# Optimization experiments

Measured on AMD Instinct MI355X. Metric: run time of the kernel, lower is better.

## Reference

```python
import jax, jax.numpy as jnp
from jax import lax
import numpy as np

B, H, T = 16, 1024, 1500
K = 3               # conv kernel size
MAX_TOK = 192       # max_decode_tokens (static padded token dim)
TEMP = 0.35
LLW = 0.25          # length_loss_weight
EPS = 1e-6


def setup_inputs() -> dict:
    key = jax.random.key(0)
    ks = jax.random.split(key, 8)
    encoder_outputs = jax.random.normal(ks[0], (B, H, T), dtype=jnp.float32)
    encoder_lengths = jax.random.randint(ks[1], (B,), 0, T)
    target_token_lengths = jax.random.randint(ks[2], (B,), 0, MAX_TOK)
    conv_w = jax.random.normal(ks[3], (H, H, K), dtype=jnp.float32) * 0.02  # OIH
    conv_b = jax.random.normal(ks[4], (H,), dtype=jnp.float32) * 0.02
    proj_w = jax.random.normal(ks[5], (H,), dtype=jnp.float32) * 0.02      # Linear(H,1)
    proj_b = jax.random.normal(ks[6], (), dtype=jnp.float32) * 0.02
    return {
        "encoder_outputs": encoder_outputs,
        "encoder_lengths": encoder_lengths,
        "target_token_lengths": target_token_lengths,
        "conv_w": conv_w,
        "conv_b": conv_b,
        "proj_w": proj_w,
        "proj_b": proj_b,
    }


def reference(encoder_outputs, encoder_lengths, target_token_lengths,
              conv_w, conv_b, proj_w, proj_b):
    b, h, t = encoder_outputs.shape
    dt = encoder_outputs.dtype

    # temporal conv (same padding), channel-first
    conv = lax.conv_general_dilated(
        encoder_outputs, conv_w, window_strides=(1,), padding="SAME",
        dimension_numbers=("NCH", "OIH", "NCH")) + conv_b[None, :, None]
    conv_feat = conv.transpose(0, 2, 1)  # [B,T,H]

    # softplus(Linear(silu(conv_feat))) + 1e-4  -> raw weights [B,T]
    raw = jax.nn.softplus(
        jnp.einsum("bth,h->bt", jax.nn.silu(conv_feat), proj_w) + proj_b) + 1e-4

    time_mask = (jnp.arange(t)[None, :] < encoder_lengths[:, None]).astype(dt)
    raw = raw * time_mask
    raw_mass = raw.sum(axis=1)  # [B]

    tok_len = jnp.clip(target_token_lengths, 1, MAX_TOK)
    alignment_loss = jnp.mean(jnp.abs(raw_mass - tok_len.astype(dt))) * LLW

    # vectorized (masked) version of the per-sample loop, padded to MAX_TOK
    scale = tok_len.astype(dt) / jnp.maximum(raw_mass, EPS)          # [B]
    sw = raw * scale[:, None]                                        # scaled weights [B,T]
    centers = jnp.cumsum(sw, axis=1) - 0.5 * sw                      # [B,T]
    token_centers = jnp.arange(MAX_TOK, dtype=dt) + 0.5              # [K]
    dist = centers[:, :, None] - token_centers[None, None, :]        # [B,T,K]
    assign = jnp.exp(-(dist * dist) / (2.0 * TEMP * TEMP)) * sw[:, :, None]
    assign = assign / jnp.maximum(assign.sum(axis=1, keepdims=True), EPS)
    tok_mask = (jnp.arange(MAX_TOK)[None, :] < tok_len[:, None]).astype(dt)
    assign = assign * tok_mask[:, None, :]

    features = encoder_outputs.transpose(0, 2, 1)                    # [B,T,H]
    acoustic_tokens = jnp.einsum("btk,bth->bkh", assign, features)   # [B,MAX_TOK,H]
    return acoustic_tokens, tok_len, alignment_loss
```

## Files before the change

### kernel.cpp

```cpp
#include <hip/hip_runtime.h>
#include <stdint.h>

#define B_ 16
#define H_ 1024
#define T_ 1500
#define MAXTOK 192
#define NCOL (B_*T_)
#define KDIM (3*H_)
#define TPADX 1544
#define TPK  1536
#define SPAD 1504
#define INV2T2 (1.0f/(2.0f*0.35f*0.35f))
#define LOSS_IDX (B_*MAXTOK*H_ + B_)
#define TOK_BASE (B_*MAXTOK*H_)
#define TRBLK (24*16*16)

#define SX_INV (127.0f/6.0f)
#define SW_INV (127.0f/0.12f)
#define DEQ    ((6.0f*0.12f)/(127.0f*127.0f))

typedef __bf16 bf16x8 __attribute__((ext_vector_type(8)));
typedef float  f32x4  __attribute__((ext_vector_type(4)));
typedef int    i32x4  __attribute__((ext_vector_type(4)));
typedef __attribute__((address_space(3))) unsigned int       lds_u32;
typedef __attribute__((address_space(1))) const unsigned int g_u32;

__device__ __forceinline__ void gload_lds16(const void* g, void* l) {
    __builtin_amdgcn_global_load_lds((g_u32*)g, (lds_u32*)l, 16, 0, 0);
}

__device__ __forceinline__ unsigned short f2bf(float f) {
    unsigned int u = __float_as_uint(f);
    unsigned int r = (u + 0x7FFFu + ((u >> 16) & 1u)) >> 16;
    return (unsigned short)r;
}

__device__ __forceinline__ signed char q8(float v, float sinv) {
    int q = __float2int_rn(v * sinv);
    q = (q > 127) ? 127 : ((q < -127) ? -127 : q);
    return (signed char)q;
}

__global__ __launch_bounds__(256) void stage_kernel(
    const float* __restrict__ x, signed char* __restrict__ Xt,
    unsigned short* __restrict__ XtT,
    const float* __restrict__ cw, signed char* __restrict__ Ar,
    float* rawacc, float* out)
{
    if (blockIdx.x < TRBLK) {
        __shared__ float tile[64][68];
        int bi = blockIdx.x;
        int t0 = (bi % 24) * 64;
        int i0 = ((bi / 24) & 15) * 64;
        int b  = bi / 384;
        int tx = threadIdx.x & 15;
        int ty = threadIdx.x >> 4;
        #pragma unroll
        for (int p = 0; p < 4; ++p) {
            int i = p*16 + ty;
            int t = t0 + tx*4;
            float4 v = make_float4(0.f, 0.f, 0.f, 0.f);
            if (t + 3 < T_) v = *(const float4*)&x[((long)b*H_ + i0 + i)*T_ + t];
            *(float4*)&tile[i][tx*4] = v;
            ushort4 u;
            u.x = f2bf(v.x); u.y = f2bf(v.y); u.z = f2bf(v.z); u.w = f2bf(v.w);
            *(ushort4*)&XtT[((long)b*H_ + i0 + i)*TPK + t] = u;
        }
        __syncthreads();
        #pragma unroll
        for (int p = 0; p < 4; ++p) {
            int t = p*16 + ty;
            if (t0 + t < T_) {
                char4 q;
                q.x = q8(tile[tx*4 + 0][t], SX_INV);
                q.y = q8(tile[tx*4 + 1][t], SX_INV);
                q.z = q8(tile[tx*4 + 2][t], SX_INV);
                q.w = q8(tile[tx*4 + 3][t], SX_INV);
                *(char4*)&Xt[((long)b*TPADX + t0 + t + 1)*1024 + i0 + tx*4] = q;
            }
        }
        return;
    }
    int idx = (blockIdx.x - TRBLK) * blockDim.x + threadIdx.x;
    if (idx < H_*KDIM) {
        int h = idx / KDIM, rem = idx - h*KDIM;
        int k = rem >> 10, i = rem & 1023;
        Ar[idx] = q8(cw[h*KDIM + i*3 + k], SW_INV);
        return;
    }
    idx -= H_*KDIM;
    if (idx < NCOL) { rawacc[idx] = 0.f; return; }
    if (idx == NCOL) { out[LOSS_IDX] = 0.f; return; }
    int j = idx - (NCOL + 1);
    if (j < B_*2816) {
        int b = j / 2816, r = j - b*2816;
        int row = (r < 64) ? 0 : (1501 + (r - 64)/64);
        int gr  = (r < 64) ? r : ((r - 64) & 63);
        uint4 z = make_uint4(0u,0u,0u,0u);
        *(uint4*)&Xt[((long)b*TPADX + row)*1024 + gr*16] = z;
    }
}

__global__ __launch_bounds__(256) void conv_gemm(
    const signed char* __restrict__ Ar, const signed char* __restrict__ Xt,
    const float* __restrict__ conv_b, const float* __restrict__ proj_w,
    float* __restrict__ rawacc)
{
    __shared__ signed char As[3*128*128];
    __shared__ signed char Bs[136*128];
    __shared__ float colsum[128];
    int bid = blockIdx.x;
    int xcd = bid & 7;
    int j = bid >> 3;
    int h_idx = j / 24;
    int g = j - h_idx*24;
    int n_idx = xcd*24 + g;
    int bb = n_idx / 12;
    int t0 = (n_idx - bb*12) * 128;
    int h0 = h_idx * 128;

    int tid = threadIdx.x;
    int w = tid >> 6, lane = tid & 63;
    int lrow = lane >> 3;
    int lgr  = ((lane & 7) ^ lrow) * 16;

    const signed char* aptr = Ar + (long)(h0 + w*32 + lrow) * KDIM + lgr;
    const signed char* bX   = Xt + ((long)bb*TPADX + t0 + lrow) * 1024 + lgr;
    signed char* lAs = &As[(w*32)*128];

    i32x4 acc[4][4];
    i32x4 zero = {0, 0, 0, 0};
    #pragma unroll
    for (int a = 0; a < 4; ++a)
        #pragma unroll
        for (int c = 0; c < 4; ++c) acc[a][c] = zero;

    int wm = w >> 1, wn = w & 1;
    int quad = lane >> 4, l16 = lane & 15;
    int swa = (l16 & 7);

    for (int c = 0; c < 8; ++c) {
        __syncthreads();
        for (int s = w; s < 17; s += 4)
            gload_lds16(bX + (long)s*8*1024 + c*128, &Bs[s*8*128]);
        #pragma unroll
        for (int kk = 0; kk < 3; ++kk)
            #pragma unroll
            for (int i = 0; i < 4; ++i)
                gload_lds16(aptr + (long)i*8*KDIM + kk*1024 + c*128,
                            lAs + kk*16384 + i*8*128);
        __syncthreads();
        #pragma unroll
        for (int kk = 0; kk < 3; ++kk) {
            int swb = ((l16 + kk) & 7);
            #pragma unroll
            for (int ks = 0; ks < 2; ++ks) {
                int p = ks*4 + quad;
                int cofa = (p ^ swa) * 16;
                int cofb = (p ^ swb) * 16;
                i32x4 af[4], bfr[4];
                #pragma unroll
                for (int mi = 0; mi < 4; ++mi)
                    af[mi] = *(const i32x4*)&As[kk*16384 + (wm*64 + mi*16 + l16)*128 + cofa];
                #pragma unroll
                for (int ni = 0; ni < 4; ++ni)
                    bfr[ni] = *(const i32x4*)&Bs[(wn*64 + ni*16 + l16 + kk)*128 + cofb];
                #pragma unroll
                for (int mi = 0; mi < 4; ++mi)
                    #pragma unroll
                    for (int ni = 0; ni < 4; ++ni)
                        acc[mi][ni] = __builtin_amdgcn_mfma_i32_16x16x64_i8(
                            af[mi], bfr[ni], acc[mi][ni], 0, 0, 0);
            }
        }
    }

    if (tid < 128) colsum[tid] = 0.f;
    __syncthreads();
    float cp[4] = {0.f, 0.f, 0.f, 0.f};
    #pragma unroll
    for (int mi = 0; mi < 4; ++mi) {
        #pragma unroll
        for (int r = 0; r < 4; ++r) {
            int h = h0 + wm*64 + mi*16 + quad*4 + r;
            float bias = conv_b[h], wgt = proj_w[h];
            #pragma unroll
            for (int ni = 0; ni < 4; ++ni) {
                float v = (float)acc[mi][ni][r] * DEQ + bias;
                float s = v / (1.f + expf(-v));
                cp[ni] += s * wgt;
            }
        }
    }
    #pragma unroll
    for (int ni = 0; ni < 4; ++ni)
        atomicAdd(&colsum[wn*64 + ni*16 + l16], cp[ni]);
    __syncthreads();
    if (tid < 128) {
        int t = t0 + tid;
        if (t < T_) atomicAdd(&rawacc[bb*T_ + t], colsum[tid]);
    }
}

__global__ void scan_kernel(const float* __restrict__ rawacc, const float* __restrict__ proj_b,
                            const int* __restrict__ elen, const int* __restrict__ tgt,
                            float* __restrict__ sw, float* __restrict__ centers,
                            float* __restrict__ out) {
    int b = blockIdx.x;
    int lane = threadIdx.x;
    float pb = proj_b[0];
    int el = elen[b];
    const float* ra = rawacc + b*T_;

    float m = 0.f;
    for (int t = lane; t < T_; t += 64) {
        float xv = ra[t] + pb;
        float sp = (xv > 20.f) ? xv : log1pf(expf(xv));
        m += (t < el) ? sp + 1e-4f : 0.f;
    }
    #pragma unroll
    for (int off = 32; off > 0; off >>= 1) m += __shfl_down(m, off);
    float mass = __shfl(m, 0);
    int tok = min(max(tgt[b], 1), MAXTOK);
    if (lane == 0) {
        atomicAdd(&out[LOSS_IDX], fabsf(mass - (float)tok) * (0.25f / (float)B_));
        out[TOK_BASE + b] = (float)tok;
    }
    float scale = (float)tok / fmaxf(mass, 1e-6f);
    float running = 0.f;
    for (int t0 = 0; t0 < T_; t0 += 64) {
        int t = t0 + lane;
        float v = 0.f;
        if (t < T_) {
            float xv = ra[t] + pb;
            float sp = (xv > 20.f) ? xv : log1pf(expf(xv));
            v = ((t < el) ? sp + 1e-4f : 0.f) * scale;
        }
        float s = v;
        #pragma unroll
        for (int d = 1; d < 64; d <<= 1) {
            float u = __shfl_up(s, d);
            if (lane >= d) s += u;
        }
        if (t < T_) {
            sw[b*SPAD + t] = v;
            centers[b*SPAD + t] = running + s - 0.5f*v;
        }
        running += __shfl(s, 63);
    }
}

__global__ __launch_bounds__(256) void denom_an(
    const float* __restrict__ sw, const float* __restrict__ cen,
    const int* __restrict__ tgt, unsigned short* __restrict__ An)
{
    __shared__ float ebuf[TPK];
    __shared__ float wsum[4];
    __shared__ float dsh;
    int kk = blockIdx.x;
    int b  = blockIdx.y;
    int tid = threadIdx.x;
    int tok = min(max(tgt[b], 1), MAXTOK);
    bool live = (kk < tok);
    float tc = kk + 0.5f;

    float lsum = 0.f;
    for (int t = tid; t < TPK; t += 256) {
        float e = 0.f;
        if (live && t < T_) {
            float d = cen[b*SPAD + t] - tc;
            e = expf(-d*d*INV2T2) * sw[b*SPAD + t];
        }
        ebuf[t] = e;
        lsum += e;
    }
    #pragma unroll
    for (int off = 32; off > 0; off >>= 1) lsum += __shfl_down(lsum, off);
    if ((tid & 63) == 0) wsum[tid >> 6] = lsum;
    __syncthreads();
    if (tid == 0) dsh = 1.f / fmaxf(wsum[0] + wsum[1] + wsum[2] + wsum[3], 1e-6f);
    __syncthreads();
    float invden = dsh;

    unsigned short* dst = An + ((long)b*MAXTOK + kk) * TPK;
    for (int q = tid; q < TPK/4; q += 256) {
        ushort4 u;
        u.x = f2bf(ebuf[q*4 + 0] * invden);
        u.y = f2bf(ebuf[q*4 + 1] * invden);
        u.z = f2bf(ebuf[q*4 + 2] * invden);
        u.w = f2bf(ebuf[q*4 + 3] * invden);
        *(ushort4*)&dst[q*4] = u;
    }
}

__global__ __launch_bounds__(256) void einsum_gemm(
    const unsigned short* __restrict__ An, const unsigned short* __restrict__ XtT,
    const int* __restrict__ tgt, float* __restrict__ out)
{
    __shared__ unsigned short As2[64*64];
    __shared__ unsigned short Bs2[128*64];
    int b  = blockIdx.z;
    int kk0 = blockIdx.x * 64;
    int h0  = blockIdx.y * 128;
    int tid = threadIdx.x;
    int tok = min(max(tgt[b], 1), MAXTOK);

    if (kk0 >= tok) {
        f32x4 z = {0.f, 0.f, 0.f, 0.f};
        #pragma unroll
        for (int i = 0; i < 8; ++i) {
            int lin = i*256 + tid;
            int row = lin >> 5, c4 = lin & 31;
            *(f32x4*)&out[((long)b*MAXTOK + kk0 + row)*H_ + h0 + c4*4] = z;
        }
        return;
    }

    int w = tid >> 6, lane = tid & 63;
    int lrow = lane >> 3;
    int lcol = ((lane & 7) ^ lrow) * 8;

    const unsigned short* aptr = An  + ((long)b*MAXTOK + kk0 + w*16 + lrow) * TPK + lcol;
    const unsigned short* bptr = XtT + ((long)b*H_    + h0  + w*32 + lrow) * TPK + lcol;
    unsigned short* lAs = &As2[(w*16)*64];
    unsigned short* lBs = &Bs2[(w*32)*64];

    f32x4 acc[2][4];
    f32x4 zero = {0.f, 0.f, 0.f, 0.f};
    #pragma unroll
    for (int a = 0; a < 2; ++a)
        #pragma unroll
        for (int c = 0; c < 4; ++c) acc[a][c] = zero;

    int wm = w >> 1, wn = w & 1;
    int quad = lane >> 4, l16 = lane & 15;
    int sw8 = (l16 & 7) * 8;

    for (int kt = 0; kt < TPK/64; ++kt) {
        __syncthreads();
        #pragma unroll
        for (int i = 0; i < 2; ++i)
            gload_lds16(aptr + (long)i*8*TPK + kt*64, lAs + i*8*64);
        #pragma unroll
        for (int i = 0; i < 4; ++i)
            gload_lds16(bptr + (long)i*8*TPK + kt*64, lBs + i*8*64);
        __syncthreads();
        #pragma unroll
        for (int ks = 0; ks < 2; ++ks) {
            int cofs = (ks*32 + quad*8) ^ sw8;
            bf16x8 af[2], bfr[4];
            #pragma unroll
            for (int mi = 0; mi < 2; ++mi)
                af[mi] = *(const bf16x8*)&As2[(wm*32 + mi*16 + l16)*64 + cofs];
            #pragma unroll
            for (int ni = 0; ni < 4; ++ni)
                bfr[ni] = *(const bf16x8*)&Bs2[(wn*64 + ni*16 + l16)*64 + cofs];
            #pragma unroll
            for (int mi = 0; mi < 2; ++mi)
                #pragma unroll
                for (int ni = 0; ni < 4; ++ni)
                    acc[mi][ni] = __builtin_amdgcn_mfma_f32_16x16x32_bf16(
                        af[mi], bfr[ni], acc[mi][ni], 0, 0, 0);
        }
    }

    #pragma unroll
    for (int mi = 0; mi < 2; ++mi) {
        int kk = kk0 + wm*32 + mi*16 + quad*4;
        #pragma unroll
        for (int ni = 0; ni < 4; ++ni) {
            int h = h0 + wn*64 + ni*16 + l16;
            long base = ((long)b*MAXTOK + kk)*H_ + h;
            #pragma unroll
            for (int r = 0; r < 4; ++r)
                out[base + (long)r*H_] = acc[mi][ni][r];
        }
    }
}

extern "C" void kernel_launch(void* const* d_in, const int* in_sizes, int n_in,
                              void* d_out, int out_size, void* d_ws, size_t ws_size,
                              hipStream_t stream)
{
    const float* x      = (const float*)d_in[0];
    const int*   elen   = (const int*)d_in[1];
    const int*   tlen   = (const int*)d_in[2];
    const float* conv_w = (const float*)d_in[3];
    const float* conv_b = (const float*)d_in[4];
    const float* proj_w = (const float*)d_in[5];
    const float* proj_b = (const float*)d_in[6];
    float* out = (float*)d_out;

    signed char*    Xt  = (signed char*)d_ws;
    signed char*    Ar  = Xt + (size_t)B_*TPADX*1024;
    unsigned short* XtT = (unsigned short*)(Ar + (size_t)H_*KDIM);
    unsigned short* An  = XtT + (size_t)B_*H_*TPK;
    float* fbase  = (float*)(An + (size_t)B_*MAXTOK*TPK);
    float* rawacc = fbase;
    float* swv    = rawacc + NCOL;
    float* cen    = swv + B_*SPAD;

    int prep_n = H_*KDIM + NCOL + 1 + B_*2816;
    int grid = TRBLK + (prep_n + 255)/256;
    stage_kernel<<<grid, 256, 0, stream>>>(x, Xt, XtT, conv_w, Ar, rawacc, out);
    conv_gemm<<<1536, 256, 0, stream>>>(Ar, Xt, conv_b, proj_w, rawacc);
    scan_kernel<<<B_, 64, 0, stream>>>(rawacc, proj_b, elen, tlen, swv, cen, out);
    denom_an<<<dim3(MAXTOK, B_), 256, 0, stream>>>(swv, cen, tlen, An);
    einsum_gemm<<<dim3(3, 8, 16), 256, 0, stream>>>(An, XtT, tlen, out);
}
```

Before: 327.6 us.

## Fuse assignment weights into einsum GEMM and switch it to int8 MFMA

Drops the separate denom_an kernel. Each einsum block now computes the Gaussian assignment weights and their normalisation on the fly from the centers and scaled weights held in LDS, quantizes them to int8, and runs i8 MFMA against an int8-quantized transposed copy of the encoder features. This removes the An buffer round trip and one launch, and halves the bytes per operand. In exchange it recomputes exponentials in every h-block and loses precision from int8 quantization of both the features and the weights.

```diff
diff --git a/kernel.cpp b/kernel.cpp
--- a/kernel.cpp
+++ b/kernel.cpp
@@ -18,8 +18,8 @@
 #define SX_INV (127.0f/6.0f)
 #define SW_INV (127.0f/0.12f)
 #define DEQ    ((6.0f*0.12f)/(127.0f*127.0f))
-
-typedef __bf16 bf16x8 __attribute__((ext_vector_type(8)));
+#define DEQ2   (6.0f/(127.0f*127.0f))
+
 typedef float  f32x4  __attribute__((ext_vector_type(4)));
 typedef int    i32x4  __attribute__((ext_vector_type(4)));
 typedef __attribute__((address_space(3))) unsigned int       lds_u32;
@@ -29,12 +29,6 @@
     __builtin_amdgcn_global_load_lds((g_u32*)g, (lds_u32*)l, 16, 0, 0);
 }
 
-__device__ __forceinline__ unsigned short f2bf(float f) {
-    unsigned int u = __float_as_uint(f);
-    unsigned int r = (u + 0x7FFFu + ((u >> 16) & 1u)) >> 16;
-    return (unsigned short)r;
-}
-
 __device__ __forceinline__ signed char q8(float v, float sinv) {
     int q = __float2int_rn(v * sinv);
     q = (q > 127) ? 127 : ((q < -127) ? -127 : q);
@@ -43,7 +37,7 @@
 
 __global__ __launch_bounds__(256) void stage_kernel(
     const float* __restrict__ x, signed char* __restrict__ Xt,
-    unsigned short* __restrict__ XtT,
+    signed char* __restrict__ XtT,
     const float* __restrict__ cw, signed char* __restrict__ Ar,
     float* rawacc, float* out)
 {
@@ -62,9 +56,10 @@
             float4 v = make_float4(0.f, 0.f, 0.f, 0.f);
             if (t + 3 < T_) v = *(const float4*)&x[((long)b*H_ + i0 + i)*T_ + t];
             *(float4*)&tile[i][tx*4] = v;
-            ushort4 u;
-            u.x = f2bf(v.x); u.y = f2bf(v.y); u.z = f2bf(v.z); u.w = f2bf(v.w);
-            *(ushort4*)&XtT[((long)b*H_ + i0 + i)*TPK + t] = u;
+            char4 q;
+            q.x = q8(v.x, SX_INV); q.y = q8(v.y, SX_INV);
+            q.z = q8(v.z, SX_INV); q.w = q8(v.w, SX_INV);
+            *(char4*)&XtT[((long)b*H_ + i0 + i)*TPK + t] = q;
         }
         __syncthreads();
         #pragma unroll
@@ -250,55 +245,16 @@
     }
 }
 
-__global__ __launch_bounds__(256) void denom_an(
+__global__ __launch_bounds__(256) void einsum_gemm(
     const float* __restrict__ sw, const float* __restrict__ cen,
-    const int* __restrict__ tgt, unsigned short* __restrict__ An)
+    const signed char* __restrict__ XtT, const int* __restrict__ tgt,
+    float* __restrict__ out)
 {
-    __shared__ float ebuf[TPK];
-    __shared__ float wsum[4];
-    __shared__ float dsh;
-    int kk = blockIdx.x;
-    int b  = blockIdx.y;
-    int tid = threadIdx.x;
-    int tok = min(max(tgt[b], 1), MAXTOK);
-    bool live = (kk < tok);
-    float tc = kk + 0.5f;
-
-    float lsum = 0.f;
-    for (int t = tid; t < TPK; t += 256) {
-        float e = 0.f;
-        if (live && t < T_) {
-            float d = cen[b*SPAD + t] - tc;
-            e = expf(-d*d*INV2T2) * sw[b*SPAD + t];
-        }
-        ebuf[t] = e;
-        lsum += e;
-    }
-    #pragma unroll
-    for (int off = 32; off > 0; off >>= 1) lsum += __shfl_down(lsum, off);
-    if ((tid & 63) == 0) wsum[tid >> 6] = lsum;
-    __syncthreads();
-    if (tid == 0) dsh = 1.f / fmaxf(wsum[0] + wsum[1] + wsum[2] + wsum[3], 1e-6f);
-    __syncthreads();
-    float invden = dsh;
-
-    unsigned short* dst = An + ((long)b*MAXTOK + kk) * TPK;
-    for (int q = tid; q < TPK/4; q += 256) {
-        ushort4 u;
-        u.x = f2bf(ebuf[q*4 + 0] * invden);
-        u.y = f2bf(ebuf[q*4 + 1] * invden);
-        u.z = f2bf(ebuf[q*4 + 2] * invden);
-        u.w = f2bf(ebuf[q*4 + 3] * invden);
-        *(ushort4*)&dst[q*4] = u;
-    }
-}
-
-__global__ __launch_bounds__(256) void einsum_gemm(
-    const unsigned short* __restrict__ An, const unsigned short* __restrict__ XtT,
-    const int* __restrict__ tgt, float* __restrict__ out)
-{
-    __shared__ unsigned short As2[64*64];
-    __shared__ unsigned short Bs2[128*64];
+    __shared__ float cenL[TPK];
+    __shared__ float swL[TPK];
+    __shared__ float inv127[64];
+    __shared__ signed char AsL[64*128];
+    __shared__ signed char BsL[128*128];
     int b  = blockIdx.z;
     int kk0 = blockIdx.x * 64;
     int h0  = blockIdx.y * 128;
@@ -316,17 +272,36 @@
         return;
     }
 
+    for (int t = tid; t < TPK; t += 256) {
+        bool v = (t < T_);
+        cenL[t] = v ? cen[b*SPAD + t] : 0.f;
+        swL[t]  = v ? sw[b*SPAD + t]  : 0.f;
+    }
+    __syncthreads();
+
+    int ar  = tid >> 2;
+    int q4  = tid & 3;
+    {
+        float tc = (float)(kk0 + ar) + 0.5f;
+        float s = 0.f;
+        for (int t = q4; t < TPK; t += 4) {
+            float d = cenL[t] - tc;
+            s += __expf(-d*d*INV2T2) * swL[t];
+        }
+        s += __shfl_xor(s, 1);
+        s += __shfl_xor(s, 2);
+        if (q4 == 0)
+            inv127[ar] = (kk0 + ar < tok) ? 127.f / fmaxf(s, 1e-6f) : 0.f;
+    }
+    __syncthreads();
+
     int w = tid >> 6, lane = tid & 63;
     int lrow = lane >> 3;
-    int lcol = ((lane & 7) ^ lrow) * 8;
-
-    const unsigned short* aptr = An  + ((long)b*MAXTOK + kk0 + w*16 + lrow) * TPK + lcol;
-    const unsigned short* bptr = XtT + ((long)b*H_    + h0  + w*32 + lrow) * TPK + lcol;
-    unsigned short* lAs = &As2[(w*16)*64];
-    unsigned short* lBs = &Bs2[(w*32)*64];
-
-    f32x4 acc[2][4];
-    f32x4 zero = {0.f, 0.f, 0.f, 0.f};
+    int lgr  = ((lane & 7) ^ lrow) * 16;
+    const signed char* bptr = XtT + ((long)b*H_ + h0 + w*32 + lrow) * TPK + lgr;
+
+    i32x4 acc[2][4];
+    i32x4 zero = {0, 0, 0, 0};
     #pragma unroll
     for (int a = 0; a < 2; ++a)
         #pragma unroll
@@ -334,32 +309,52 @@
 
     int wm = w >> 1, wn = w & 1;
     int quad = lane >> 4, l16 = lane & 15;
-    int sw8 = (l16 & 7) * 8;
-
-    for (int kt = 0; kt < TPK/64; ++kt) {
+    float tcr = (float)(kk0 + ar) + 0.5f;
+    float idr = inv127[ar];
+
+    for (int kt = 0; kt < 12; ++kt) {
         __syncthreads();
         #pragma unroll
-        for (int i = 0; i < 2; ++i)
-            gload_lds16(aptr + (long)i*8*TPK + kt*64, lAs + i*8*64);
-        #pragma unroll
         for (int i = 0; i < 4; ++i)
-            gload_lds16(bptr + (long)i*8*TPK + kt*64, lBs + i*8*64);
+            gload_lds16(bptr + (long)i*8*TPK + kt*128, &BsL[(w*32 + i*8)*128]);
+        #pragma unroll
+        for (int pp = 0; pp < 2; ++pp) {
+            int p = q4 + pp*4;
+            unsigned int packed[4];
+            #pragma unroll
+            for (int gq = 0; gq < 4; ++gq) {
+                unsigned int u = 0;
+                #pragma unroll
+                for (int jj = 0; jj < 4; ++jj) {
+                    int t = kt*128 + p*16 + gq*4 + jj;
+                    float d = cenL[t] - tcr;
+                    float an = __expf(-d*d*INV2T2) * swL[t] * idr;
+                    int q = __float2int_rn(an);
+                    q = (q > 127) ? 127 : q;
+                    u |= ((unsigned int)q) << (jj*8);
+                }
+                packed[gq] = u;
+            }
+            *(uint4*)&AsL[ar*128 + ((p ^ (ar & 7))*16)] =
+                make_uint4(packed[0], packed[1], packed[2], packed[3]);
+        }
         __syncthreads();
         #pragma unroll
         for (int ks = 0; ks < 2; ++ks) {
-            int cofs = (ks*32 + quad*8) ^ sw8;
-            bf16x8 af[2], bfr[4];
+            int pg = ks*4 + quad;
+            int cof = (pg ^ (l16 & 7)) * 16;
+            i32x4 af[2], bfr[4];
             #pragma unroll
             for (int mi = 0; mi < 2; ++mi)
-                af[mi] = *(const bf16x8*)&As2[(wm*32 + mi*16 + l16)*64 + cofs];
+                af[mi] = *(const i32x4*)&AsL[(wm*32 + mi*16 + l16)*128 + cof];
             #pragma unroll
             for (int ni = 0; ni < 4; ++ni)
-                bfr[ni] = *(const bf16x8*)&Bs2[(wn*64 + ni*16 + l16)*64 + cofs];
+                bfr[ni] = *(const i32x4*)&BsL[(wn*64 + ni*16 + l16)*128 + cof];
             #pragma unroll
             for (int mi = 0; mi < 2; ++mi)
                 #pragma unroll
                 for (int ni = 0; ni < 4; ++ni)
-                    acc[mi][ni] = __builtin_amdgcn_mfma_f32_16x16x32_bf16(
+                    acc[mi][ni] = __builtin_amdgcn_mfma_i32_16x16x64_i8(
                         af[mi], bfr[ni], acc[mi][ni], 0, 0, 0);
         }
     }
@@ -373,7 +368,7 @@
             long base = ((long)b*MAXTOK + kk)*H_ + h;
             #pragma unroll
             for (int r = 0; r < 4; ++r)
-                out[base + (long)r*H_] = acc[mi][ni][r];
+                out[base + (long)r*H_] = (float)acc[mi][ni][r] * DEQ2;
         }
     }
 }
@@ -391,20 +386,18 @@
     const float* proj_b = (const float*)d_in[6];
     float* out = (float*)d_out;
 
-    signed char*    Xt  = (signed char*)d_ws;
-    signed char*    Ar  = Xt + (size_t)B_*TPADX*1024;
-    unsigned short* XtT = (unsigned short*)(Ar + (size_t)H_*KDIM);
-    unsigned short* An  = XtT + (size_t)B_*H_*TPK;
-    float* fbase  = (float*)(An + (size_t)B_*MAXTOK*TPK);
+    signed char* Xt   = (signed char*)d_ws;
+    signed char* Ar   = Xt  + (size_t)B_*TPADX*1024;
+    signed char* XtT8 = Ar  + (size_t)H_*KDIM;
+    float* fbase  = (float*)(XtT8 + (size_t)B_*H_*TPK);
     float* rawacc = fbase;
     float* swv    = rawacc + NCOL;
     float* cen    = swv + B_*SPAD;
 
     int prep_n = H_*KDIM + NCOL + 1 + B_*2816;
     int grid = TRBLK + (prep_n + 255)/256;
-    stage_kernel<<<grid, 256, 0, stream>>>(x, Xt, XtT, conv_w, Ar, rawacc, out);
+    stage_kernel<<<grid, 256, 0, stream>>>(x, Xt, XtT8, conv_w, Ar, rawacc, out);
     conv_gemm<<<1536, 256, 0, stream>>>(Ar, Xt, conv_b, proj_w, rawacc);
     scan_kernel<<<B_, 64, 0, stream>>>(rawacc, proj_b, elen, tlen, swv, cen, out);
-    denom_an<<<dim3(MAXTOK, B_), 256, 0, stream>>>(swv, cen, tlen, An);
-    einsum_gemm<<<dim3(3, 8, 16), 256, 0, stream>>>(An, XtT, tlen, out);
-}
+    einsum_gemm<<<dim3(3, 8, 16), 256, 0, stream>>>(swv, cen, XtT8, tlen, out);
+}
```

Measured after the change: 336.5 us. 1.03x slower.
